# Optimization experiments

Hardware: AMD Instinct MI355X
Metric: run time of the kernel (lower is better)

## Reference

```python
import jax, jax.numpy as jnp
import numpy as np

RES = [64, 128, 256, 512, 1024]   # per-level grid resolutions
NF = 8                            # n_features per level
NC = 2                            # n_cells (staggered grid copies)
P = 1_000_000                     # number of query points


def setup_inputs() -> dict:
    key = jax.random.key(0)
    ks = jax.random.split(key, 2 + len(RES))
    x = jax.random.uniform(ks[0], (P, 1), dtype=jnp.float32)
    y = jax.random.uniform(ks[1], (P, 1), dtype=jnp.float32)
    inp = {"x": x, "y": y}
    for i, r in enumerate(RES):
        # F_active[i]: uniform in [-1e-5, 1e-5], shape (n_cells, n_features, r, r)
        inp[f"table{i}"] = jax.random.uniform(
            ks[2 + i], (NC, NF, r, r), dtype=jnp.float32, minval=-1e-5, maxval=1e-5)
    return inp


def _sample_level(table, xn, yn):
    """Manual bilinear grid_sample (align_corners=True) with per-cell staggered
    sub-pixel offsets (offset=True in the original grid_sample_2d).
    table: (nc, C, H, W); xn, yn: (P,) in [-1, 1]. Returns (P, C)."""
    nc, C, H, W = table.shape
    off = jnp.arange(nc, dtype=xn.dtype) / nc              # staggered offsets in pixels
    ix = (xn + 1.0) * 0.5 * (W - 1) + off[:, None]         # (nc, P) pixel coords
    iy = (yn + 1.0) * 0.5 * (H - 1) + off[:, None]
    x0 = jnp.floor(ix)
    y0 = jnp.floor(iy)
    wx = ix - x0                                            # bilinear weights (nc, P)
    wy = iy - y0
    x0i = jnp.clip(x0.astype(jnp.int32), 0, W - 1)
    x1i = jnp.clip(x0i + 1, 0, W - 1)
    y0i = jnp.clip(y0.astype(jnp.int32), 0, H - 1)
    y1i = jnp.clip(y0i + 1, 0, H - 1)

    def per_cell(tab, x0i, x1i, y0i, y1i, wx, wy):
        t = tab.reshape(C, H * W)                           # (C, HW)
        g = lambda yi, xi: t[:, yi * W + xi]                # gather -> (C, P)
        nw = g(y0i, x0i); ne = g(y0i, x1i)
        sw = g(y1i, x0i); se = g(y1i, x1i)
        return (nw * (1 - wx) * (1 - wy) + ne * wx * (1 - wy)
                + sw * (1 - wx) * wy + se * wx * wy)        # (C, P)

    feats = jax.vmap(per_cell)(table, x0i, x1i, y0i, y1i, wx, wy)  # (nc, C, P)
    return feats.sum(0).T                                   # sum over cells -> (P, C)


def reference(x, y, table0, table1, table2, table3, table4):
    # domain_size = [0,1,0,1] -> normalize to [-1, 1]
    xn = (x * 2.0 - 1.0)[:, 0]
    yn = (y * 2.0 - 1.0)[:, 0]
    tables = [table0, table1, table2, table3, table4]
    # concat per-level features along feature dim -> (P, NF * len(RES))
    return jnp.concatenate([_sample_level(t, xn, yn) for t in tables], axis=1)
```

## Files before the change

kernel.cpp:

```cpp
#include <hip/hip_runtime.h>


#define WS_PART 64
#define WS_CURS 24576
#define WS_OVFC 40960
#define WS_OVF 65536
#define WS_PERM 2162688
#define WS_SXY 7143424
#define WS_TAB 17301504
#define WS_END_BF16 61997056ull
#define WS_END_I8 39649280ull
#define NGRP 4096
#define CAP 304
#define OVF_CAP 524288
#define LDS_CAP 1600

typedef __attribute__((ext_vector_type(8))) unsigned short ushort8v;

__device__ __forceinline__ unsigned short f2bf(float f) {
  union { float f; unsigned u; } c; c.f = f;
  unsigned u = c.u;
  u += 0x7FFFu + ((u >> 16) & 1u);
  return (unsigned short)(u >> 16);
}

__device__ __forceinline__ void scatter_one(
    const float* __restrict__ x, const float* __restrict__ y, int p,
    unsigned* __restrict__ cursor, unsigned* __restrict__ ovf_cnt,
    int* __restrict__ ovf, int* __restrict__ perm, float2* __restrict__ sxy) {
  float xv = x[p], yv = y[p];
  int bx = min(max((int)(xv * 128.0f), 0), 127);
  int by = min(max((int)(yv * 128.0f), 0), 127);
  int g = (by >> 1) * 64 + (bx >> 1);
  unsigned s = atomicAdd(&cursor[g], 1u);
  if (s < CAP) {
    int slot = g * CAP + (int)s;
    perm[slot] = p;
    sxy[slot] = make_float2(xv * 2.0f - 1.0f, yv * 2.0f - 1.0f);
  } else {
    unsigned o = atomicAdd(ovf_cnt, 1u);
    if (o < OVF_CAP) ovf[o] = p;
  }
}

__global__ __launch_bounds__(256) void transform_scatter_kernel(
    const float* __restrict__ s0, const float* __restrict__ s1,
    const float* __restrict__ s2, const float* __restrict__ s3,
    const float* __restrict__ s4, uint4* __restrict__ tb,
    const float* __restrict__ x, const float* __restrict__ y, int P,
    unsigned* __restrict__ cursor, unsigned* __restrict__ ovf_cnt,
    int* __restrict__ ovf, int* __restrict__ perm, float2* __restrict__ sxy) {
  int b = blockIdx.x;
  if (b >= 10912) {
    int stride = (gridDim.x - 10912) * 256;
    for (int p = (b - 10912) * 256 + (int)threadIdx.x; p < P; p += stride)
      scatter_one(x, y, p, cursor, ovf_cnt, ovf, perm, sxy);
    return;
  }
  const float* src; int HW; int lb; size_t toff;
  if (b < 32)        { src = s0; HW = 4096;    lb = 0;    toff = 0; }
  else if (b < 160)  { src = s1; HW = 16384;   lb = 32;   toff = 8192; }
  else if (b < 672)  { src = s2; HW = 65536;   lb = 160;  toff = 40960; }
  else if (b < 2720) { src = s3; HW = 262144;  lb = 672;  toff = 172032; }
  else               { src = s4; HW = 1048576; lb = 2720; toff = 696320; }
  int i = (b - lb) * 256 + (int)threadIdx.x;
  int cell = i / HW;
  int pix = i - cell * HW;
  const float* s = src + (size_t)cell * 8u * (size_t)HW + (size_t)pix;
  ushort8v v;
#pragma unroll
  for (int ch = 0; ch < 8; ++ch) v[ch] = f2bf(s[(size_t)ch * HW]);
  ((ushort8v*)tb)[toff + (size_t)i] = v;
}

struct Win { int ixmin, iymin, ww, wh, base; };

template <int W>
__device__ __forceinline__ Win mkwin(float xlo, float xhi, float ylo, float yhi,
                                     int base) {
  const float s = (float)(W - 1);
  Win w;
  w.ixmin = max(0, (int)floorf(xlo * s) - 1);
  int ixmax = min(W - 1, (int)floorf(xhi * s + 0.5f) + 2);
  w.iymin = max(0, (int)floorf(ylo * s) - 1);
  int iymax = min(W - 1, (int)floorf(yhi * s + 0.5f) + 2);
  w.ww = ixmax - w.ixmin + 1;
  w.wh = iymax - w.iymin + 1;
  w.base = base;
  return w;
}

__device__ __forceinline__ void store8(float* __restrict__ o,
                                       const float* __restrict__ r) {
  ((float4*)o)[0] = make_float4(r[0], r[1], r[2], r[3]);
  ((float4*)o)[1] = make_float4(r[4], r[5], r[6], r[7]);
}

template <int W>
__device__ __forceinline__ void stage_bf16(uint4* __restrict__ lds, const Win& w,
                                           const uint4* __restrict__ t) {
  int n = w.ww * w.wh;
  for (int j = (int)threadIdx.x; j < 2 * n; j += 256) {
    int cell = j >= n;
    int jj = cell ? j - n : j;
    int r = jj / w.ww;
    int c = jj - r * w.ww;
    lds[w.base + j] = t[cell * W * W + (w.iymin + r) * W + (w.ixmin + c)];
  }
}

__device__ __forceinline__ void fma_bf(uint4 v, float w, float* __restrict__ acc) {
  acc[0] = fmaf(__uint_as_float(v.x << 16), w, acc[0]);
  acc[1] = fmaf(__uint_as_float(v.x & 0xFFFF0000u), w, acc[1]);
  acc[2] = fmaf(__uint_as_float(v.y << 16), w, acc[2]);
  acc[3] = fmaf(__uint_as_float(v.y & 0xFFFF0000u), w, acc[3]);
  acc[4] = fmaf(__uint_as_float(v.z << 16), w, acc[4]);
  acc[5] = fmaf(__uint_as_float(v.z & 0xFFFF0000u), w, acc[5]);
  acc[6] = fmaf(__uint_as_float(v.w << 16), w, acc[6]);
  acc[7] = fmaf(__uint_as_float(v.w & 0xFFFF0000u), w, acc[7]);
}

template <int W>
__device__ __forceinline__ void sample_bf_lds(const uint4* __restrict__ lds,
                                              const Win& w, float xn, float yn,
                                              float* __restrict__ res) {
  const float s = (float)(W - 1);
  float acc[8];
#pragma unroll
  for (int i = 0; i < 8; ++i) acc[i] = 0.0f;
#pragma unroll
  for (int cell = 0; cell < 2; ++cell) {
    const float off = 0.5f * (float)cell;
    float ix = (xn + 1.0f) * 0.5f * s + off;
    float iy = (yn + 1.0f) * 0.5f * s + off;
    float xf = floorf(ix), yf = floorf(iy);
    float wx = ix - xf, wy = iy - yf;
    int x0 = min(max((int)xf, 0), W - 1);
    int y0 = min(max((int)yf, 0), W - 1);
    int x1 = min(x0 + 1, W - 1);
    int y1 = min(y0 + 1, W - 1);
    int cb = w.base + cell * (w.ww * w.wh) - w.ixmin;
    int r0 = cb + (y0 - w.iymin) * w.ww;
    int r1 = cb + (y1 - w.iymin) * w.ww;
    uint4 c00 = lds[r0 + x0], c01 = lds[r0 + x1];
    uint4 c10 = lds[r1 + x0], c11 = lds[r1 + x1];
    float w00 = (1.0f - wx) * (1.0f - wy);
    float w01 = wx * (1.0f - wy);
    float w10 = (1.0f - wx) * wy;
    float w11 = wx * wy;
    fma_bf(c00, w00, acc);
    fma_bf(c01, w01, acc);
    fma_bf(c10, w10, acc);
    fma_bf(c11, w11, acc);
  }
#pragma unroll
  for (int i = 0; i < 8; ++i) res[i] = acc[i];
}

template <int W>
__device__ __forceinline__ void sample_bf_glob(const uint4* __restrict__ t,
                                               float xn, float yn,
                                               float* __restrict__ res) {
  const float s = (float)(W - 1);
  float acc[8];
#pragma unroll
  for (int i = 0; i < 8; ++i) acc[i] = 0.0f;
#pragma unroll
  for (int cell = 0; cell < 2; ++cell) {
    const float off = 0.5f * (float)cell;
    float ix = (xn + 1.0f) * 0.5f * s + off;
    float iy = (yn + 1.0f) * 0.5f * s + off;
    float xf = floorf(ix), yf = floorf(iy);
    float wx = ix - xf, wy = iy - yf;
    int x0 = min(max((int)xf, 0), W - 1);
    int y0 = min(max((int)yf, 0), W - 1);
    int x1 = min(x0 + 1, W - 1);
    int y1 = min(y0 + 1, W - 1);
    const uint4* b = t + cell * W * W;
    uint4 c00 = b[y0 * W + x0], c01 = b[y0 * W + x1];
    uint4 c10 = b[y1 * W + x0], c11 = b[y1 * W + x1];
    float w00 = (1.0f - wx) * (1.0f - wy);
    float w01 = wx * (1.0f - wy);
    float w10 = (1.0f - wx) * wy;
    float w11 = wx * wy;
    fma_bf(c00, w00, acc);
    fma_bf(c01, w01, acc);
    fma_bf(c10, w10, acc);
    fma_bf(c11, w11, acc);
  }
#pragma unroll
  for (int i = 0; i < 8; ++i) res[i] = acc[i];
}

__global__ __launch_bounds__(256) void sample_tile_bf16(
    const float2* __restrict__ sxy, const int* __restrict__ perm,
    const unsigned* __restrict__ cursor, const unsigned* __restrict__ ovf_cnt,
    const int* __restrict__ ovf,
    const float* __restrict__ x, const float* __restrict__ y,
    const uint4* __restrict__ t0, const uint4* __restrict__ t1,
    const uint4* __restrict__ t2, const uint4* __restrict__ t3,
    const uint4* __restrict__ t4, float* __restrict__ out, int P) {
  __shared__ uint4 lds[LDS_CAP];
  int g = blockIdx.x;

  if (g >= NGRP) {
    int n = min((int)*ovf_cnt, OVF_CAP);
    int stride = (gridDim.x - NGRP) * 256;
    for (int i = (g - NGRP) * 256 + (int)threadIdx.x; i < n; i += stride) {
      int p = ovf[i];
      float xn = x[p] * 2.0f - 1.0f;
      float yn = y[p] * 2.0f - 1.0f;
      float* orow = out + (size_t)p * 40u;
      float res[8];
      sample_bf_glob<64>(t0, xn, yn, res);   store8(orow + 0, res);
      sample_bf_glob<128>(t1, xn, yn, res);  store8(orow + 8, res);
      sample_bf_glob<256>(t2, xn, yn, res);  store8(orow + 16, res);
      sample_bf_glob<512>(t3, xn, yn, res);  store8(orow + 24, res);
      sample_bf_glob<1024>(t4, xn, yn, res); store8(orow + 32, res);
    }
    return;
  }

  int cnt = min((int)cursor[g], CAP);
  if (cnt == 0) return;

  int gx = g & 63, gy = g >> 6;
  float xlo = (float)gx * (1.0f / 64.0f);
  float xhi = (float)(gx + 1) * (1.0f / 64.0f);
  float ylo = (float)gy * (1.0f / 64.0f);
  float yhi = (float)(gy + 1) * (1.0f / 64.0f);

  Win w0 = mkwin<64>(xlo, xhi, ylo, yhi, 0);
  Win w1 = mkwin<128>(xlo, xhi, ylo, yhi, w0.base + 2 * w0.ww * w0.wh);
  Win w2 = mkwin<256>(xlo, xhi, ylo, yhi, w1.base + 2 * w1.ww * w1.wh);
  Win w3 = mkwin<512>(xlo, xhi, ylo, yhi, w2.base + 2 * w2.ww * w2.wh);
  Win w4 = mkwin<1024>(xlo, xhi, ylo, yhi, w3.base + 2 * w3.ww * w3.wh);
  int total = w4.base + 2 * w4.ww * w4.wh;
  bool use_lds = (total <= LDS_CAP);

  if (use_lds) {
    stage_bf16<64>(lds, w0, t0);
    stage_bf16<128>(lds, w1, t1);
    stage_bf16<256>(lds, w2, t2);
    stage_bf16<512>(lds, w3, t3);
    stage_bf16<1024>(lds, w4, t4);
    __syncthreads();
  }

  const float2* gsxy = sxy + g * CAP;
  const int* gperm = perm + g * CAP;
  for (int i = (int)threadIdx.x; i < cnt; i += 256) {
    float2 c = gsxy[i];
    int q = gperm[i];
    float xn = c.x, yn = c.y;
    float* orow = out + (size_t)q * 40u;
    float res[8];
    if (use_lds) {
      sample_bf_lds<64>(lds, w0, xn, yn, res);   store8(orow + 0, res);
      sample_bf_lds<128>(lds, w1, xn, yn, res);  store8(orow + 8, res);
      sample_bf_lds<256>(lds, w2, xn, yn, res);  store8(orow + 16, res);
      sample_bf_lds<512>(lds, w3, xn, yn, res);  store8(orow + 24, res);
      sample_bf_lds<1024>(lds, w4, xn, yn, res); store8(orow + 32, res);
    } else {
      sample_bf_glob<64>(t0, xn, yn, res);   store8(orow + 0, res);
      sample_bf_glob<128>(t1, xn, yn, res);  store8(orow + 8, res);
      sample_bf_glob<256>(t2, xn, yn, res);  store8(orow + 16, res);
      sample_bf_glob<512>(t3, xn, yn, res);  store8(orow + 24, res);
      sample_bf_glob<1024>(t4, xn, yn, res); store8(orow + 32, res);
    }
  }
}

__global__ __launch_bounds__(256) void absmax_scatter_kernel(
    const float* __restrict__ s0, const float* __restrict__ s1,
    const float* __restrict__ s2, const float* __restrict__ s3,
    const float* __restrict__ s4, unsigned* __restrict__ partials,
    const float* __restrict__ x, const float* __restrict__ y, int P,
    unsigned* __restrict__ cursor, unsigned* __restrict__ ovf_cnt,
    int* __restrict__ ovf, int* __restrict__ perm, float2* __restrict__ sxy) {
  int b = blockIdx.x;
  if (b >= 5456) {
    int stride = (gridDim.x - 5456) * 256;
    for (int p = (b - 5456) * 256 + (int)threadIdx.x; p < P; p += stride)
      scatter_one(x, y, p, cursor, ovf_cnt, ovf, perm, sxy);
    return;
  }
  __shared__ unsigned red[4];
  const float* src; int n4; int lb; int nb;
  if (b < 16)        { src = s0; n4 = 16384;   lb = 0;    nb = 16; }
  else if (b < 80)   { src = s1; n4 = 65536;   lb = 16;   nb = 64; }
  else if (b < 336)  { src = s2; n4 = 262144;  lb = 80;   nb = 256; }
  else if (b < 1360) { src = s3; n4 = 1048576; lb = 336;  nb = 1024; }
  else               { src = s4; n4 = 4194304; lb = 1360; nb = 4096; }
  int local = b - lb;
  unsigned m = 0;
  for (int k = local * 256 + threadIdx.x; k < n4; k += nb * 256) {
    float4 v = ((const float4*)src)[k];
    unsigned a = __float_as_uint(v.x) & 0x7FFFFFFFu;
    unsigned c = __float_as_uint(v.y) & 0x7FFFFFFFu;
    unsigned d = __float_as_uint(v.z) & 0x7FFFFFFFu;
    unsigned e = __float_as_uint(v.w) & 0x7FFFFFFFu;
    m = max(m, max(max(a, c), max(d, e)));
  }
#pragma unroll
  for (int off = 32; off; off >>= 1)
    m = max(m, (unsigned)__shfl_xor((int)m, off));
  if ((threadIdx.x & 63) == 0) red[threadIdx.x >> 6] = m;
  __syncthreads();
  if (threadIdx.x == 0)
    partials[b] = max(max(red[0], red[1]), max(red[2], red[3]));
}

__global__ __launch_bounds__(256) void finalize_scales_kernel(
    const unsigned* __restrict__ partials, float* __restrict__ deq,
    float* __restrict__ inv) {
  __shared__ unsigned red[4];
  int t = (int)threadIdx.x;
  const int lo[5] = {0, 16, 80, 336, 1360};
  const int hi[5] = {16, 80, 336, 1360, 5456};
  for (int l = 0; l < 5; ++l) {
    unsigned m = 0;
    for (int i = lo[l] + t; i < hi[l]; i += 256) m = max(m, partials[i]);
#pragma unroll
    for (int off = 32; off; off >>= 1)
      m = max(m, (unsigned)__shfl_xor((int)m, off));
    if ((t & 63) == 0) red[t >> 6] = m;
    __syncthreads();
    if (t == 0) {
      unsigned r = max(max(red[0], red[1]), max(red[2], red[3]));
      float s = __uint_as_float(r);
      if (!(s > 0.0f)) s = 1e-20f;
      deq[l] = s / 127.0f;
      inv[l] = 127.0f / s;
    }
    __syncthreads();
  }
}

__global__ __launch_bounds__(256) void quant_kernel(
    const float* __restrict__ s0, const float* __restrict__ s1,
    const float* __restrict__ s2, const float* __restrict__ s3,
    const float* __restrict__ s4, uint2* __restrict__ tb,
    const float* __restrict__ invp) {
  int b = blockIdx.x;
  const float* src; int HW; int lb; int l; size_t toff;
  if (b < 32)        { src = s0; HW = 4096;    lb = 0;    l = 0; toff = 0; }
  else if (b < 160)  { src = s1; HW = 16384;   lb = 32;   l = 1; toff = 8192; }
  else if (b < 672)  { src = s2; HW = 65536;   lb = 160;  l = 2; toff = 40960; }
  else if (b < 2720) { src = s3; HW = 262144;  lb = 672;  l = 3; toff = 172032; }
  else               { src = s4; HW = 1048576; lb = 2720; l = 4; toff = 696320; }
  int i = (b - lb) * 256 + (int)threadIdx.x;
  float sc = invp[l];
  int cell = i / HW;
  int pix = i - cell * HW;
  const float* s = src + (size_t)cell * 8u * (size_t)HW + (size_t)pix;
  unsigned lov = 0, hiv = 0;
#pragma unroll
  for (int c = 0; c < 4; ++c) {
    int q = (int)rintf(s[(size_t)c * HW] * sc);
    q = min(max(q, -127), 127);
    lov |= ((unsigned)(q & 0xFF)) << (8 * c);
  }
#pragma unroll
  for (int c = 0; c < 4; ++c) {
    int q = (int)rintf(s[(size_t)(c + 4) * HW] * sc);
    q = min(max(q, -127), 127);
    hiv |= ((unsigned)(q & 0xFF)) << (8 * c);
  }
  tb[toff + (size_t)i] = make_uint2(lov, hiv);
}

template <int W>
__device__ __forceinline__ void stage_i8(uint2* __restrict__ lds, const Win& w,
                                         const uint2* __restrict__ t) {
  int n = w.ww * w.wh;
  for (int i = (int)threadIdx.x; i < 2 * n; i += 256) {
    int cell = i >= n;
    int j = cell ? i - n : i;
    int r = j / w.ww;
    int c = j - r * w.ww;
    lds[w.base + i] = t[cell * W * W + (w.iymin + r) * W + (w.ixmin + c)];
  }
}

__device__ __forceinline__ void fma_i8(unsigned lo, unsigned hi, float w,
                                       float* __restrict__ acc) {
#pragma unroll
  for (int c = 0; c < 4; ++c)
    acc[c] = fmaf((float)(signed char)(lo >> (8 * c)), w, acc[c]);
#pragma unroll
  for (int c = 0; c < 4; ++c)
    acc[4 + c] = fmaf((float)(signed char)(hi >> (8 * c)), w, acc[4 + c]);
}

template <int W>
__device__ __forceinline__ void sample_i8(const uint2* __restrict__ lds,
                                          const Win& w, bool use_lds,
                                          const uint2* __restrict__ t,
                                          float xn, float yn, float deq,
                                          float* __restrict__ res) {
  const float s = (float)(W - 1);
  float acc[8];
#pragma unroll
  for (int i = 0; i < 8; ++i) acc[i] = 0.0f;
#pragma unroll
  for (int cell = 0; cell < 2; ++cell) {
    const float off = 0.5f * (float)cell;
    float ix = (xn + 1.0f) * 0.5f * s + off;
    float iy = (yn + 1.0f) * 0.5f * s + off;
    float xf = floorf(ix), yf = floorf(iy);
    float wx = ix - xf, wy = iy - yf;
    int x0 = min(max((int)xf, 0), W - 1);
    int y0 = min(max((int)yf, 0), W - 1);
    int x1 = min(x0 + 1, W - 1);
    int y1 = min(y0 + 1, W - 1);
    uint2 c00, c01, c10, c11;
    if (use_lds) {
      int cb = w.base + cell * (w.ww * w.wh) - w.ixmin;
      int r0 = cb + (y0 - w.iymin) * w.ww;
      int r1 = cb + (y1 - w.iymin) * w.ww;
      c00 = lds[r0 + x0]; c01 = lds[r0 + x1];
      c10 = lds[r1 + x0]; c11 = lds[r1 + x1];
    } else {
      const uint2* b = t + cell * W * W;
      c00 = b[y0 * W + x0]; c01 = b[y0 * W + x1];
      c10 = b[y1 * W + x0]; c11 = b[y1 * W + x1];
    }
    float w00 = (1.0f - wx) * (1.0f - wy);
    float w01 = wx * (1.0f - wy);
    float w10 = (1.0f - wx) * wy;
    float w11 = wx * wy;
    fma_i8(c00.x, c00.y, w00, acc);
    fma_i8(c01.x, c01.y, w01, acc);
    fma_i8(c10.x, c10.y, w10, acc);
    fma_i8(c11.x, c11.y, w11, acc);
  }
#pragma unroll
  for (int i = 0; i < 8; ++i) res[i] = acc[i] * deq;
}

__global__ __launch_bounds__(256) void sample_tile_i8(
    const float2* __restrict__ sxy, const int* __restrict__ perm,
    const unsigned* __restrict__ cursor, const unsigned* __restrict__ ovf_cnt,
    const int* __restrict__ ovf,
    const float* __restrict__ x, const float* __restrict__ y,
    const uint2* __restrict__ t0, const uint2* __restrict__ t1,
    const uint2* __restrict__ t2, const uint2* __restrict__ t3,
    const uint2* __restrict__ t4, const float* __restrict__ deqs,
    float* __restrict__ out, int P) {
  __shared__ uint2 lds[LDS_CAP];
  int g = blockIdx.x;
  float d0 = deqs[0], d1 = deqs[1], d2 = deqs[2], d3 = deqs[3], d4 = deqs[4];
  Win wdum = {0, 0, 1, 1, 0};

  if (g >= NGRP) {
    int n = min((int)*ovf_cnt, OVF_CAP);
    int stride = (gridDim.x - NGRP) * 256;
    for (int i = (g - NGRP) * 256 + (int)threadIdx.x; i < n; i += stride) {
      int p = ovf[i];
      float xn = x[p] * 2.0f - 1.0f;
      float yn = y[p] * 2.0f - 1.0f;
      float* orow = out + (size_t)p * 40u;
      float res[8];
      sample_i8<64>(lds, wdum, false, t0, xn, yn, d0, res);   store8(orow + 0, res);
      sample_i8<128>(lds, wdum, false, t1, xn, yn, d1, res);  store8(orow + 8, res);
      sample_i8<256>(lds, wdum, false, t2, xn, yn, d2, res);  store8(orow + 16, res);
      sample_i8<512>(lds, wdum, false, t3, xn, yn, d3, res);  store8(orow + 24, res);
      sample_i8<1024>(lds, wdum, false, t4, xn, yn, d4, res); store8(orow + 32, res);
    }
    return;
  }

  int cnt = min((int)cursor[g], CAP);
  if (cnt == 0) return;

  int gx = g & 63, gy = g >> 6;
  float xlo = (float)gx * (1.0f / 64.0f);
  float xhi = (float)(gx + 1) * (1.0f / 64.0f);
  float ylo = (float)gy * (1.0f / 64.0f);
  float yhi = (float)(gy + 1) * (1.0f / 64.0f);

  Win w0 = mkwin<64>(xlo, xhi, ylo, yhi, 0);
  Win w1 = mkwin<128>(xlo, xhi, ylo, yhi, w0.base + 2 * w0.ww * w0.wh);
  Win w2 = mkwin<256>(xlo, xhi, ylo, yhi, w1.base + 2 * w1.ww * w1.wh);
  Win w3 = mkwin<512>(xlo, xhi, ylo, yhi, w2.base + 2 * w2.ww * w2.wh);
  Win w4 = mkwin<1024>(xlo, xhi, ylo, yhi, w3.base + 2 * w3.ww * w3.wh);
  int total = w4.base + 2 * w4.ww * w4.wh;
  bool use_lds = (total <= LDS_CAP);

  if (use_lds) {
    stage_i8<64>(lds, w0, t0);
    stage_i8<128>(lds, w1, t1);
    stage_i8<256>(lds, w2, t2);
    stage_i8<512>(lds, w3, t3);
    stage_i8<1024>(lds, w4, t4);
    __syncthreads();
  }

  const float2* gsxy = sxy + g * CAP;
  const int* gperm = perm + g * CAP;
  for (int i = (int)threadIdx.x; i < cnt; i += 256) {
    float2 c = gsxy[i];
    int q = gperm[i];
    float xn = c.x, yn = c.y;
    float* orow = out + (size_t)q * 40u;
    float res[8];
    sample_i8<64>(lds, w0, use_lds, t0, xn, yn, d0, res);   store8(orow + 0, res);
    sample_i8<128>(lds, w1, use_lds, t1, xn, yn, d1, res);  store8(orow + 8, res);
    sample_i8<256>(lds, w2, use_lds, t2, xn, yn, d2, res);  store8(orow + 16, res);
    sample_i8<512>(lds, w3, use_lds, t3, xn, yn, d3, res);  store8(orow + 24, res);
    sample_i8<1024>(lds, w4, use_lds, t4, xn, yn, d4, res); store8(orow + 32, res);
  }
}

template <int W>
__device__ __forceinline__ void sample_level_direct(
    const float* __restrict__ t, float xv, float yv, float* __restrict__ o) {
  float acc[8];
#pragma unroll
  for (int i = 0; i < 8; ++i) acc[i] = 0.0f;
  float xn = xv * 2.0f - 1.0f;
  float yn = yv * 2.0f - 1.0f;
#pragma unroll
  for (int cell = 0; cell < 2; ++cell) {
    const float off = 0.5f * (float)cell;
    float ix = (xn + 1.0f) * 0.5f * (float)(W - 1) + off;
    float iy = (yn + 1.0f) * 0.5f * (float)(W - 1) + off;
    float x0f = floorf(ix), y0f = floorf(iy);
    float wx = ix - x0f, wy = iy - y0f;
    int x0 = (int)x0f; x0 = min(max(x0, 0), W - 1);
    int y0 = (int)y0f; y0 = min(max(y0, 0), W - 1);
    int x1 = min(x0 + 1, W - 1);
    int y1 = min(y0 + 1, W - 1);
    float w00 = (1.0f - wx) * (1.0f - wy);
    float w01 = wx * (1.0f - wy);
    float w10 = (1.0f - wx) * wy;
    float w11 = wx * wy;
    size_t i00 = (size_t)y0 * W + x0;
    size_t i01 = (size_t)y0 * W + x1;
    size_t i10 = (size_t)y1 * W + x0;
    size_t i11 = (size_t)y1 * W + x1;
#pragma unroll
    for (int c = 0; c < 8; ++c) {
      const float* pc = t + (size_t)cell * 8u * (size_t)W * (size_t)W +
                        (size_t)c * (size_t)W * (size_t)W;
      acc[c] += pc[i00] * w00 + pc[i01] * w01 + pc[i10] * w10 + pc[i11] * w11;
    }
  }
#pragma unroll
  for (int i = 0; i < 8; ++i) o[i] = acc[i];
}

__global__ __launch_bounds__(256) void sample_kernel_direct(
    const float* __restrict__ x, const float* __restrict__ y,
    const float* __restrict__ t0, const float* __restrict__ t1,
    const float* __restrict__ t2, const float* __restrict__ t3,
    const float* __restrict__ t4, float* __restrict__ out, int P) {
  int p = blockIdx.x * blockDim.x + threadIdx.x;
  if (p >= P) return;
  float xv = x[p];
  float yv = y[p];
  float o[8];
  float* orow = out + (size_t)p * 40u;
  sample_level_direct<64>(t0, xv, yv, o);
#pragma unroll
  for (int i = 0; i < 8; ++i) orow[0 + i] = o[i];
  sample_level_direct<128>(t1, xv, yv, o);
#pragma unroll
  for (int i = 0; i < 8; ++i) orow[8 + i] = o[i];
  sample_level_direct<256>(t2, xv, yv, o);
#pragma unroll
  for (int i = 0; i < 8; ++i) orow[16 + i] = o[i];
  sample_level_direct<512>(t3, xv, yv, o);
#pragma unroll
  for (int i = 0; i < 8; ++i) orow[24 + i] = o[i];
  sample_level_direct<1024>(t4, xv, yv, o);
#pragma unroll
  for (int i = 0; i < 8; ++i) orow[32 + i] = o[i];
}

extern "C" void kernel_launch(void* const* d_in, const int* in_sizes, int n_in,
                              void* d_out, int out_size, void* d_ws, size_t ws_size,
                              hipStream_t stream) {
  const float* x = (const float*)d_in[0];
  const float* y = (const float*)d_in[1];
  const float* tabs[5] = {(const float*)d_in[2], (const float*)d_in[3],
                          (const float*)d_in[4], (const float*)d_in[5],
                          (const float*)d_in[6]};
  float* out = (float*)d_out;
  const int P = in_sizes[0];

  const size_t offs[5] = {0, 8192, 40960, 172032, 696320};

  unsigned* cursor = (unsigned*)((char*)d_ws + WS_CURS);
  unsigned* ovf_cnt = (unsigned*)((char*)d_ws + WS_OVFC);
  int* ovf = (int*)((char*)d_ws + WS_OVF);
  int* perm = (int*)((char*)d_ws + WS_PERM);
  float2* sxy = (float2*)((char*)d_ws + WS_SXY);

  if (ws_size >= WS_END_BF16 && P <= 1000448) {
    uint4* tb = (uint4*)((char*)d_ws + WS_TAB);
    (void)hipMemsetAsync((char*)d_ws + WS_CURS, 0, (WS_OVFC - WS_CURS) + 4,
                         stream);
    transform_scatter_kernel<<<10912 + 2048, 256, 0, stream>>>(
        tabs[0], tabs[1], tabs[2], tabs[3], tabs[4], tb, x, y, P, cursor,
        ovf_cnt, ovf, perm, sxy);
    sample_tile_bf16<<<NGRP + 32, 256, 0, stream>>>(
        sxy, perm, cursor, ovf_cnt, ovf, x, y, tb + offs[0], tb + offs[1],
        tb + offs[2], tb + offs[3], tb + offs[4], out, P);
  } else if (ws_size >= WS_END_I8 && P <= 1000448) {
    float* deq = (float*)d_ws;
    float* inv = (float*)((char*)d_ws + 32);
    unsigned* partials = (unsigned*)((char*)d_ws + WS_PART);
    uint2* tb = (uint2*)((char*)d_ws + WS_TAB);
    (void)hipMemsetAsync((char*)d_ws + WS_CURS, 0, (WS_OVFC - WS_CURS) + 4,
                         stream);
    absmax_scatter_kernel<<<5456 + 2048, 256, 0, stream>>>(
        tabs[0], tabs[1], tabs[2], tabs[3], tabs[4], partials, x, y, P, cursor,
        ovf_cnt, ovf, perm, sxy);
    finalize_scales_kernel<<<1, 256, 0, stream>>>(partials, deq, inv);
    quant_kernel<<<10912, 256, 0, stream>>>(
        tabs[0], tabs[1], tabs[2], tabs[3], tabs[4], tb, inv);
    sample_tile_i8<<<NGRP + 32, 256, 0, stream>>>(
        sxy, perm, cursor, ovf_cnt, ovf, x, y, tb + offs[0], tb + offs[1],
        tb + offs[2], tb + offs[3], tb + offs[4], deq, out, P);
  } else {
    sample_kernel_direct<<<(P + 255) / 256, 256, 0, stream>>>(
        x, y, tabs[0], tabs[1], tabs[2], tabs[3], tabs[4], out, P);
  }
}
```

Before: 199.3 us.

## Interleave bucketed point data into packed slots and launch scatter blocks first

Replaces the separate perm and sxy bucket arrays with one interleaved 12-byte record (xn, yn, point index) per slot, so scatter and sample touch one stream instead of two. Scatter blocks are moved to the front of the combined grid and doubled to 4096 in the bf16 path so they get dispatched early. The workspace is also repacked and the overflow cap is reduced. The 12-byte stride gives unaligned, non-vector loads, and the smaller overflow buffer leaves less headroom for crowded buckets.

```diff
diff --git a/kernel.cpp b/kernel.cpp
--- a/kernel.cpp
+++ b/kernel.cpp
@@ -1,19 +1,22 @@
 #include <hip/hip_runtime.h>
 
 
-#define WS_PART 64
-#define WS_CURS 24576
-#define WS_OVFC 40960
+#define WS_CURS 0
+#define WS_OVFC 16384
+#define WS_DEQ 16448
+#define WS_INV 16480
+#define WS_PART 20480
 #define WS_OVF 65536
-#define WS_PERM 2162688
-#define WS_SXY 7143424
-#define WS_TAB 17301504
-#define WS_END_BF16 61997056ull
-#define WS_END_I8 39649280ull
+#define WS_SLOT 589824
+#define WS_TAB 15532032
+#define WS_END_BF16 60227584ull
+#define WS_END_I8 37879808ull
 #define NGRP 4096
 #define CAP 304
-#define OVF_CAP 524288
+#define OVF_CAP 131072
 #define LDS_CAP 1600
+#define NSCAT_BF16 4096
+#define NSCAT_I8 2048
 
 typedef __attribute__((ext_vector_type(8))) unsigned short ushort8v;
 
@@ -27,16 +30,17 @@
 __device__ __forceinline__ void scatter_one(
     const float* __restrict__ x, const float* __restrict__ y, int p,
     unsigned* __restrict__ cursor, unsigned* __restrict__ ovf_cnt,
-    int* __restrict__ ovf, int* __restrict__ perm, float2* __restrict__ sxy) {
+    int* __restrict__ ovf, float* __restrict__ slots) {
   float xv = x[p], yv = y[p];
   int bx = min(max((int)(xv * 128.0f), 0), 127);
   int by = min(max((int)(yv * 128.0f), 0), 127);
   int g = (by >> 1) * 64 + (bx >> 1);
   unsigned s = atomicAdd(&cursor[g], 1u);
   if (s < CAP) {
-    int slot = g * CAP + (int)s;
-    perm[slot] = p;
-    sxy[slot] = make_float2(xv * 2.0f - 1.0f, yv * 2.0f - 1.0f);
+    float* sp = slots + ((size_t)g * CAP + s) * 3u;
+    sp[0] = xv * 2.0f - 1.0f;
+    sp[1] = yv * 2.0f - 1.0f;
+    sp[2] = __int_as_float(p);
   } else {
     unsigned o = atomicAdd(ovf_cnt, 1u);
     if (o < OVF_CAP) ovf[o] = p;
@@ -49,21 +53,22 @@
     const float* __restrict__ s4, uint4* __restrict__ tb,
     const float* __restrict__ x, const float* __restrict__ y, int P,
     unsigned* __restrict__ cursor, unsigned* __restrict__ ovf_cnt,
-    int* __restrict__ ovf, int* __restrict__ perm, float2* __restrict__ sxy) {
+    int* __restrict__ ovf, float* __restrict__ slots) {
   int b = blockIdx.x;
-  if (b >= 10912) {
-    int stride = (gridDim.x - 10912) * 256;
-    for (int p = (b - 10912) * 256 + (int)threadIdx.x; p < P; p += stride)
-      scatter_one(x, y, p, cursor, ovf_cnt, ovf, perm, sxy);
+  if (b < NSCAT_BF16) {
+    int stride = NSCAT_BF16 * 256;
+    for (int p = b * 256 + (int)threadIdx.x; p < P; p += stride)
+      scatter_one(x, y, p, cursor, ovf_cnt, ovf, slots);
     return;
   }
+  int bb = b - NSCAT_BF16;
   const float* src; int HW; int lb; size_t toff;
-  if (b < 32)        { src = s0; HW = 4096;    lb = 0;    toff = 0; }
-  else if (b < 160)  { src = s1; HW = 16384;   lb = 32;   toff = 8192; }
-  else if (b < 672)  { src = s2; HW = 65536;   lb = 160;  toff = 40960; }
-  else if (b < 2720) { src = s3; HW = 262144;  lb = 672;  toff = 172032; }
-  else               { src = s4; HW = 1048576; lb = 2720; toff = 696320; }
-  int i = (b - lb) * 256 + (int)threadIdx.x;
+  if (bb < 32)        { src = s0; HW = 4096;    lb = 0;    toff = 0; }
+  else if (bb < 160)  { src = s1; HW = 16384;   lb = 32;   toff = 8192; }
+  else if (bb < 672)  { src = s2; HW = 65536;   lb = 160;  toff = 40960; }
+  else if (bb < 2720) { src = s3; HW = 262144;  lb = 672;  toff = 172032; }
+  else                { src = s4; HW = 1048576; lb = 2720; toff = 696320; }
+  int i = (bb - lb) * 256 + (int)threadIdx.x;
   int cell = i / HW;
   int pix = i - cell * HW;
   const float* s = src + (size_t)cell * 8u * (size_t)HW + (size_t)pix;
@@ -193,9 +198,8 @@
 }
 
 __global__ __launch_bounds__(256) void sample_tile_bf16(
-    const float2* __restrict__ sxy, const int* __restrict__ perm,
-    const unsigned* __restrict__ cursor, const unsigned* __restrict__ ovf_cnt,
-    const int* __restrict__ ovf,
+    const float* __restrict__ slots, const unsigned* __restrict__ cursor,
+    const unsigned* __restrict__ ovf_cnt, const int* __restrict__ ovf,
     const float* __restrict__ x, const float* __restrict__ y,
     const uint4* __restrict__ t0, const uint4* __restrict__ t1,
     const uint4* __restrict__ t2, const uint4* __restrict__ t3,
@@ -247,12 +251,11 @@
     __syncthreads();
   }
 
-  const float2* gsxy = sxy + g * CAP;
-  const int* gperm = perm + g * CAP;
+  const float* gs = slots + (size_t)g * CAP * 3u;
   for (int i = (int)threadIdx.x; i < cnt; i += 256) {
-    float2 c = gsxy[i];
-    int q = gperm[i];
-    float xn = c.x, yn = c.y;
+    const float* sp = gs + (size_t)i * 3u;
+    float xn = sp[0], yn = sp[1];
+    int q = __float_as_int(sp[2]);
     float* orow = out + (size_t)q * 40u;
     float res[8];
     if (use_lds) {
@@ -277,22 +280,23 @@
     const float* __restrict__ s4, unsigned* __restrict__ partials,
     const float* __restrict__ x, const float* __restrict__ y, int P,
     unsigned* __restrict__ cursor, unsigned* __restrict__ ovf_cnt,
-    int* __restrict__ ovf, int* __restrict__ perm, float2* __restrict__ sxy) {
+    int* __restrict__ ovf, float* __restrict__ slots) {
   int b = blockIdx.x;
-  if (b >= 5456) {
-    int stride = (gridDim.x - 5456) * 256;
-    for (int p = (b - 5456) * 256 + (int)threadIdx.x; p < P; p += stride)
-      scatter_one(x, y, p, cursor, ovf_cnt, ovf, perm, sxy);
+  if (b < NSCAT_I8) {
+    int stride = NSCAT_I8 * 256;
+    for (int p = b * 256 + (int)threadIdx.x; p < P; p += stride)
+      scatter_one(x, y, p, cursor, ovf_cnt, ovf, slots);
     return;
   }
+  int bb = b - NSCAT_I8;
   __shared__ unsigned red[4];
   const float* src; int n4; int lb; int nb;
-  if (b < 16)        { src = s0; n4 = 16384;   lb = 0;    nb = 16; }
-  else if (b < 80)   { src = s1; n4 = 65536;   lb = 16;   nb = 64; }
-  else if (b < 336)  { src = s2; n4 = 262144;  lb = 80;   nb = 256; }
-  else if (b < 1360) { src = s3; n4 = 1048576; lb = 336;  nb = 1024; }
-  else               { src = s4; n4 = 4194304; lb = 1360; nb = 4096; }
-  int local = b - lb;
+  if (bb < 16)        { src = s0; n4 = 16384;   lb = 0;    nb = 16; }
+  else if (bb < 80)   { src = s1; n4 = 65536;   lb = 16;   nb = 64; }
+  else if (bb < 336)  { src = s2; n4 = 262144;  lb = 80;   nb = 256; }
+  else if (bb < 1360) { src = s3; n4 = 1048576; lb = 336;  nb = 1024; }
+  else                { src = s4; n4 = 4194304; lb = 1360; nb = 4096; }
+  int local = bb - lb;
   unsigned m = 0;
   for (int k = local * 256 + threadIdx.x; k < n4; k += nb * 256) {
     float4 v = ((const float4*)src)[k];
@@ -308,7 +312,7 @@
   if ((threadIdx.x & 63) == 0) red[threadIdx.x >> 6] = m;
   __syncthreads();
   if (threadIdx.x == 0)
-    partials[b] = max(max(red[0], red[1]), max(red[2], red[3]));
+    partials[bb] = max(max(red[0], red[1]), max(red[2], red[3]));
 }
 
 __global__ __launch_bounds__(256) void finalize_scales_kernel(
@@ -440,9 +444,8 @@
 }
 
 __global__ __launch_bounds__(256) void sample_tile_i8(
-    const float2* __restrict__ sxy, const int* __restrict__ perm,
-    const unsigned* __restrict__ cursor, const unsigned* __restrict__ ovf_cnt,
-    const int* __restrict__ ovf,
+    const float* __restrict__ slots, const unsigned* __restrict__ cursor,
+    const unsigned* __restrict__ ovf_cnt, const int* __restrict__ ovf,
     const float* __restrict__ x, const float* __restrict__ y,
     const uint2* __restrict__ t0, const uint2* __restrict__ t1,
     const uint2* __restrict__ t2, const uint2* __restrict__ t3,
@@ -497,12 +500,11 @@
     __syncthreads();
   }
 
-  const float2* gsxy = sxy + g * CAP;
-  const int* gperm = perm + g * CAP;
+  const float* gs = slots + (size_t)g * CAP * 3u;
   for (int i = (int)threadIdx.x; i < cnt; i += 256) {
-    float2 c = gsxy[i];
-    int q = gperm[i];
-    float xn = c.x, yn = c.y;
+    const float* sp = gs + (size_t)i * 3u;
+    float xn = sp[0], yn = sp[1];
+    int q = __float_as_int(sp[2]);
     float* orow = out + (size_t)q * 40u;
     float res[8];
     sample_i8<64>(lds, w0, use_lds, t0, xn, yn, d0, res);   store8(orow + 0, res);
@@ -595,34 +597,31 @@
   unsigned* cursor = (unsigned*)((char*)d_ws + WS_CURS);
   unsigned* ovf_cnt = (unsigned*)((char*)d_ws + WS_OVFC);
   int* ovf = (int*)((char*)d_ws + WS_OVF);
-  int* perm = (int*)((char*)d_ws + WS_PERM);
-  float2* sxy = (float2*)((char*)d_ws + WS_SXY);
+  float* slots = (float*)((char*)d_ws + WS_SLOT);
 
   if (ws_size >= WS_END_BF16 && P <= 1000448) {
     uint4* tb = (uint4*)((char*)d_ws + WS_TAB);
-    (void)hipMemsetAsync((char*)d_ws + WS_CURS, 0, (WS_OVFC - WS_CURS) + 4,
-                         stream);
-    transform_scatter_kernel<<<10912 + 2048, 256, 0, stream>>>(
+    (void)hipMemsetAsync((char*)d_ws, 0, WS_OVFC + 4, stream);
+    transform_scatter_kernel<<<NSCAT_BF16 + 10912, 256, 0, stream>>>(
         tabs[0], tabs[1], tabs[2], tabs[3], tabs[4], tb, x, y, P, cursor,
-        ovf_cnt, ovf, perm, sxy);
+        ovf_cnt, ovf, slots);
     sample_tile_bf16<<<NGRP + 32, 256, 0, stream>>>(
-        sxy, perm, cursor, ovf_cnt, ovf, x, y, tb + offs[0], tb + offs[1],
+        slots, cursor, ovf_cnt, ovf, x, y, tb + offs[0], tb + offs[1],
         tb + offs[2], tb + offs[3], tb + offs[4], out, P);
   } else if (ws_size >= WS_END_I8 && P <= 1000448) {
-    float* deq = (float*)d_ws;
-    float* inv = (float*)((char*)d_ws + 32);
+    float* deq = (float*)((char*)d_ws + WS_DEQ);
+    float* inv = (float*)((char*)d_ws + WS_INV);
     unsigned* partials = (unsigned*)((char*)d_ws + WS_PART);
     uint2* tb = (uint2*)((char*)d_ws + WS_TAB);
-    (void)hipMemsetAsync((char*)d_ws + WS_CURS, 0, (WS_OVFC - WS_CURS) + 4,
-                         stream);
-    absmax_scatter_kernel<<<5456 + 2048, 256, 0, stream>>>(
+    (void)hipMemsetAsync((char*)d_ws, 0, WS_OVFC + 4, stream);
+    absmax_scatter_kernel<<<NSCAT_I8 + 5456, 256, 0, stream>>>(
         tabs[0], tabs[1], tabs[2], tabs[3], tabs[4], partials, x, y, P, cursor,
-        ovf_cnt, ovf, perm, sxy);
+        ovf_cnt, ovf, slots);
     finalize_scales_kernel<<<1, 256, 0, stream>>>(partials, deq, inv);
     quant_kernel<<<10912, 256, 0, stream>>>(
         tabs[0], tabs[1], tabs[2], tabs[3], tabs[4], tb, inv);
     sample_tile_i8<<<NGRP + 32, 256, 0, stream>>>(
-        sxy, perm, cursor, ovf_cnt, ovf, x, y, tb + offs[0], tb + offs[1],
+        slots, cursor, ovf_cnt, ovf, x, y, tb + offs[0], tb + offs[1],
         tb + offs[2], tb + offs[3], tb + offs[4], deq, out, P);
   } else {
     sample_kernel_direct<<<(P + 255) / 256, 256, 0, stream>>>(
```

New measurement: 188.6 us. 1.06x faster.
